# Optimization experiments

Measured on AMD Instinct MI355X. Metric: run time of the kernel, lower is better.

The kernel has to match this reference:

```python
import jax, jax.numpy as jnp
import numpy as np

N_NODES = 100000
N_EDGES = 3200000
D_IN = 64
D_OUT = 64


def setup_inputs() -> dict:
    key = jax.random.key(0)
    k0, k1, k2, k3 = jax.random.split(key, 4)
    x = jax.random.normal(k0, (N_NODES, D_IN), dtype=jnp.float32)
    edge_index = jax.random.randint(k1, (2, N_EDGES), 0, N_NODES, dtype=jnp.int64)
    edge_weight = jax.random.uniform(k2, (N_EDGES,), dtype=jnp.float32)
    W = jax.random.normal(k3, (D_IN, D_OUT), dtype=jnp.float32) / jnp.sqrt(jnp.float32(D_IN))
    b = jnp.zeros((D_OUT,), dtype=jnp.float32)
    return {"x": x, "edge_index": edge_index, "edge_weight": edge_weight, "W": W, "b": b}


def reference(x, edge_index, edge_weight, W, b):
    # GiGCNConv forward: asymmetric (random-walk, D^-1 A) gcn_norm with self loops,
    # then GCNConv(normalize=False): linear -> edge-weighted scatter-add -> bias.
    N = x.shape[0]
    src, dst = edge_index[0], edge_index[1]

    # add self loops (fill value 1.0 since improved=False)
    loop = jnp.arange(N, dtype=src.dtype)
    src = jnp.concatenate([src, loop])
    dst = jnp.concatenate([dst, loop])
    ew = jnp.concatenate([edge_weight.astype(x.dtype), jnp.ones((N,), dtype=x.dtype)])

    # asymmetric normalization: in-degree (at dst) inverse scaling
    deg = jax.ops.segment_sum(ew, dst, num_segments=N)          # [N]
    deg_inv = jnp.where(deg > 0, 1.0 / deg, 0.0)                # inf -> 0
    norm = deg_inv[dst] * ew                                    # [E+N]

    # GCNConv: project then aggregate messages at destination nodes
    h = x @ W                                                   # [N, D_OUT]
    msg = norm[:, None] * h[src]                                # [E+N, D_OUT] gather
    out = jax.ops.segment_sum(msg, dst, num_segments=N)         # scatter-add
    return out + b
```

## Files before the change

### kernel.cpp

```cpp
#include <hip/hip_runtime.h>


#define D 64
#define BSH 9
#define NPB 512
#define MAXB1 256
#define BATCHA 4096
#define C1S 32
#define WSCALE 8192.0f
#define WINV (1.0f / 8192.0f)

static __device__ __forceinline__ unsigned short f2bf(float f) {
    unsigned u = __float_as_uint(f);
    u += 0x7FFFu + ((u >> 16) & 1u);
    return (unsigned short)(u >> 16);
}
static __device__ __forceinline__ float bf2f(unsigned short s) {
    return __uint_as_float(((unsigned)s) << 16);
}


__global__ __launch_bounds__(256) void hist_kernel(const int* __restrict__ dst,
                                                   int* __restrict__ hist, int E, int B1) {
    __shared__ int lh[MAXB1];
    int tid = threadIdx.x;
    if (tid < MAXB1) lh[tid] = 0;
    __syncthreads();
    int t = blockIdx.x * 256 + tid;
    int stride = gridDim.x * 256;
    if ((E & 3) == 0 && (((size_t)dst & 15) == 0)) {
        const int4* d4 = (const int4*)dst;
        int n4 = E >> 2;
        for (int e = t; e < n4; e += stride) {
            int4 v = d4[e];
            atomicAdd(&lh[v.x >> BSH], 1);
            atomicAdd(&lh[v.y >> BSH], 1);
            atomicAdd(&lh[v.z >> BSH], 1);
            atomicAdd(&lh[v.w >> BSH], 1);
        }
    } else {
        for (int e = t; e < E; e += stride) {
            int d = __builtin_nontemporal_load(dst + e);
            atomicAdd(&lh[d >> BSH], 1);
        }
    }
    __syncthreads();
    if (tid < B1) {
        int v = lh[tid];
        if (v) atomicAdd(&hist[tid], v);
    }
}


__global__ __launch_bounds__(256) void scan_kernel(const int* __restrict__ hist,
                                                   int* __restrict__ off1,
                                                   int* __restrict__ cur1, int B1, int E) {
    __shared__ int s[256];
    int tid = threadIdx.x;
    int v = (tid < B1) ? hist[tid] : 0;
    s[tid] = v;
    __syncthreads();
    for (int o = 1; o < 256; o <<= 1) {
        int t = (tid >= o) ? s[tid - o] : 0;
        __syncthreads();
        s[tid] += t;
        __syncthreads();
    }
    if (tid < B1) {
        int ex = s[tid] - v;
        off1[tid] = ex;
        cur1[tid * C1S] = ex;
    }
    if (tid == 0) off1[B1] = E;
}


__global__ __launch_bounds__(256) void partA_kernel(const int* __restrict__ src,
                                                    const int* __restrict__ dst,
                                                    const float* __restrict__ ew,
                                                    int* __restrict__ cur1,
                                                    int2* __restrict__ pairs1,
                                                    int E, int nb, int aligned) {
    __shared__ int bcnt[MAXB1];
    __shared__ int bbase[MAXB1];
    __shared__ int brank[MAXB1];
    int tid = threadIdx.x;
    for (int ib = blockIdx.x; ib < nb; ib += gridDim.x) {
        int base = ib * BATCHA;
        int blen = E - base;
        if (blen > BATCHA) blen = BATCHA;
        if (tid < MAXB1) { bcnt[tid] = 0; brank[tid] = 0; }
        __syncthreads();
        int dv[16], sv[16];
        float wv[16];
        int off = tid * 16;
        if (aligned && off + 16 <= blen) {
#pragma unroll
            for (int kk = 0; kk < 4; ++kk) {
                int4 d4 = ((const int4*)(dst + base + off))[kk];
                int4 s4 = ((const int4*)(src + base + off))[kk];
                float4 w4 = ((const float4*)(ew + base + off))[kk];
                dv[kk * 4 + 0] = d4.x; dv[kk * 4 + 1] = d4.y;
                dv[kk * 4 + 2] = d4.z; dv[kk * 4 + 3] = d4.w;
                sv[kk * 4 + 0] = s4.x; sv[kk * 4 + 1] = s4.y;
                sv[kk * 4 + 2] = s4.z; sv[kk * 4 + 3] = s4.w;
                wv[kk * 4 + 0] = w4.x; wv[kk * 4 + 1] = w4.y;
                wv[kk * 4 + 2] = w4.z; wv[kk * 4 + 3] = w4.w;
            }
#pragma unroll
            for (int m = 0; m < 16; ++m) atomicAdd(&bcnt[dv[m] >> BSH], 1);
        } else {
#pragma unroll
            for (int m = 0; m < 16; ++m) {
                bool v = (off + m) < blen;
                int e = base + off + m;
                dv[m] = v ? __builtin_nontemporal_load(dst + e) : -1;
                sv[m] = v ? __builtin_nontemporal_load(src + e) : 0;
                wv[m] = v ? __builtin_nontemporal_load(ew + e) : 0.0f;
                if (v) atomicAdd(&bcnt[dv[m] >> BSH], 1);
            }
        }
        __syncthreads();
        if (tid < MAXB1 && bcnt[tid] > 0)
            bbase[tid] = atomicAdd(&cur1[tid * C1S], bcnt[tid]);
        __syncthreads();
#pragma unroll
        for (int m = 0; m < 16; ++m) {
            if (dv[m] >= 0) {
                int bin = dv[m] >> BSH;
                int r = atomicAdd(&brank[bin], 1);
                pairs1[bbase[bin] + r] =
                    make_int2(sv[m] | ((dv[m] & (NPB - 1)) << 17),
                              __float_as_int(wv[m]));
            }
        }
        __syncthreads();
    }
}


__global__ __launch_bounds__(512) void sortmerge_kernel(const int2* __restrict__ pairs1,
                                                        const int* __restrict__ off1,
                                                        unsigned* __restrict__ cw,
                                                        int* __restrict__ node_off,
                                                        int N, int B1) {
    __shared__ int lh[NPB];
    __shared__ int s[NPB];
    __shared__ int cur[NPB];
    int tid = threadIdx.x;
    int c = blockIdx.x;
    int e0 = off1[c], e1 = off1[c + 1];

    lh[tid] = 0;
    __syncthreads();

    for (int ib = e0; ib < e1; ib += 512 * 8) {
        long long pv[8];
#pragma unroll
        for (int m = 0; m < 8; ++m) {
            int i = ib + m * 512 + tid;
            pv[m] = (i < e1)
                ? __builtin_nontemporal_load((const long long*)(pairs1 + i))
                : -1LL;
        }
#pragma unroll
        for (int m = 0; m < 8; ++m) {
            int i = ib + m * 512 + tid;
            if (i < e1) atomicAdd(&lh[((int)pv[m] >> 17) & (NPB - 1)], 1);
        }
    }
    __syncthreads();

    s[tid] = lh[tid];
    __syncthreads();
    for (int o = 1; o < NPB; o <<= 1) {
        int t = (tid >= o) ? s[tid - o] : 0;
        __syncthreads();
        s[tid] += t;
        __syncthreads();
    }
    int ex = s[tid] - lh[tid];
    int gbase = c << BSH;
    if (gbase + tid <= N) node_off[gbase + tid] = e0 + ex;
    if (c == B1 - 1 && tid == 0) node_off[N] = e1;
    cur[tid] = ex;
    __syncthreads();

    for (int ib = e0; ib < e1; ib += 512 * 8) {
        long long pv[8];
#pragma unroll
        for (int m = 0; m < 8; ++m) {
            int i = ib + m * 512 + tid;
            pv[m] = (i < e1)
                ? __builtin_nontemporal_load((const long long*)(pairs1 + i))
                : -1LL;
        }
#pragma unroll
        for (int m = 0; m < 8; ++m) {
            int i = ib + m * 512 + tid;
            if (i < e1) {
                int px = (int)pv[m];
                float w = __int_as_float((int)(pv[m] >> 32));
                int node = (px >> 17) & (NPB - 1);
                int pos = atomicAdd(&cur[node], 1);
                int wq = (int)fminf(fmaxf(w, 0.0f) * WSCALE + 0.5f, 32767.0f);
                cw[e0 + pos] = (unsigned)(px & 0x1FFFF) | ((unsigned)wq << 17);
            }
        }
    }
}


__global__ __launch_bounds__(256) void gemmW_kernel(const float* __restrict__ x,
                                                    const float* __restrict__ W,
                                                    unsigned short* __restrict__ hbf, int N) {
    __shared__ float Ws[D * D];
    __shared__ float xs[32][D];
    int tid = threadIdx.x;
    int j = tid & 63;
    int g = tid >> 6;
    int base = blockIdx.x * 32;
    for (int i = tid; i < D * D; i += 256) Ws[i] = W[i];
    for (int rr = g; rr < 32; rr += 4) {
        int r = base + rr;
        if (r < N) xs[rr][j] = x[(size_t)r * D + j];
    }
    __syncthreads();
    float wc[D];
#pragma unroll
    for (int k = 0; k < D; ++k) wc[k] = Ws[k * D + j];
    for (int rr = g; rr < 32; rr += 4) {
        int r = base + rr;
        if (r < N) {
            float s0 = 0.0f, s1 = 0.0f, s2 = 0.0f, s3 = 0.0f;
#pragma unroll
            for (int k = 0; k < D; k += 4) {
                s0 = fmaf(xs[rr][k + 0], wc[k + 0], s0);
                s1 = fmaf(xs[rr][k + 1], wc[k + 1], s1);
                s2 = fmaf(xs[rr][k + 2], wc[k + 2], s2);
                s3 = fmaf(xs[rr][k + 3], wc[k + 3], s3);
            }
            hbf[(size_t)r * D + j] = f2bf((s0 + s1) + (s2 + s3));
        }
    }
}


__global__ __launch_bounds__(256) void accum_kernel(const unsigned* __restrict__ cw,
                                                    const int* __restrict__ node_off,
                                                    const unsigned short* __restrict__ hbf,
                                                    const float* __restrict__ bias,
                                                    float* __restrict__ out, int N) {
    int t = blockIdx.x * 256 + threadIdx.x;
    int n = t >> 6;
    int j = t & 63;
    if (n >= N) return;
    float acc = bf2f(hbf[(size_t)n * D + j]);
    float degs = 1.0f;
    int base = node_off[n];
    int cnt = node_off[n + 1] - base;
    const unsigned* pp = cw + base;
    int i = 0;
    for (; i + 7 < cnt; i += 8) {
        unsigned v0 = pp[i + 0];
        unsigned v1 = pp[i + 1];
        unsigned v2 = pp[i + 2];
        unsigned v3 = pp[i + 3];
        unsigned v4 = pp[i + 4];
        unsigned v5 = pp[i + 5];
        unsigned v6 = pp[i + 6];
        unsigned v7 = pp[i + 7];
        float h0 = bf2f(hbf[(size_t)(v0 & 0x1FFFF) * D + j]);
        float h1 = bf2f(hbf[(size_t)(v1 & 0x1FFFF) * D + j]);
        float h2 = bf2f(hbf[(size_t)(v2 & 0x1FFFF) * D + j]);
        float h3 = bf2f(hbf[(size_t)(v3 & 0x1FFFF) * D + j]);
        float h4 = bf2f(hbf[(size_t)(v4 & 0x1FFFF) * D + j]);
        float h5 = bf2f(hbf[(size_t)(v5 & 0x1FFFF) * D + j]);
        float h6 = bf2f(hbf[(size_t)(v6 & 0x1FFFF) * D + j]);
        float h7 = bf2f(hbf[(size_t)(v7 & 0x1FFFF) * D + j]);
        float w0 = (float)(v0 >> 17) * WINV;
        float w1 = (float)(v1 >> 17) * WINV;
        float w2 = (float)(v2 >> 17) * WINV;
        float w3 = (float)(v3 >> 17) * WINV;
        float w4 = (float)(v4 >> 17) * WINV;
        float w5 = (float)(v5 >> 17) * WINV;
        float w6 = (float)(v6 >> 17) * WINV;
        float w7 = (float)(v7 >> 17) * WINV;
        degs += ((w0 + w1) + (w2 + w3)) + ((w4 + w5) + (w6 + w7));
        acc = fmaf(w0, h0, acc);
        acc = fmaf(w1, h1, acc);
        acc = fmaf(w2, h2, acc);
        acc = fmaf(w3, h3, acc);
        acc = fmaf(w4, h4, acc);
        acc = fmaf(w5, h5, acc);
        acc = fmaf(w6, h6, acc);
        acc = fmaf(w7, h7, acc);
    }
    for (; i < cnt; ++i) {
        unsigned v = pp[i];
        float w = (float)(v >> 17) * WINV;
        degs += w;
        acc = fmaf(w, bf2f(hbf[(size_t)(v & 0x1FFFF) * D + j]), acc);
    }
    float di = (degs > 0.0f) ? (1.0f / degs) : 0.0f;
    __builtin_nontemporal_store(fmaf(di, acc, bias[j]), &out[(size_t)n * D + j]);
}


__global__ __launch_bounds__(256) void deg_kernel(const int* __restrict__ dst,
                                                  const float* __restrict__ ew,
                                                  float* __restrict__ deg, int E) {
    int t = blockIdx.x * 256 + threadIdx.x;
    int stride = gridDim.x * 256;
    for (int e = t; e < E; e += stride) atomicAdd(&deg[dst[e]], ew[e]);
}

__global__ __launch_bounds__(256) void deginv_kernel(float* __restrict__ deg, int N) {
    int t = blockIdx.x * 256 + threadIdx.x;
    int stride = gridDim.x * 256;
    for (int n = t; n < N; n += stride) {
        float tot = deg[n] + 1.0f;
        deg[n] = (tot > 0.0f) ? (1.0f / tot) : 0.0f;
    }
}

__global__ __launch_bounds__(256) void gemm16f_kernel(const float* __restrict__ x,
                                                      const float* __restrict__ W,
                                                      float* __restrict__ h, int N) {
    __shared__ float Ws[D * D];
    __shared__ float xs[16][D];
    int tid = threadIdx.x;
    int j = tid & 63;
    int q = tid >> 6;
    int base = blockIdx.x * 16;
    for (int i = tid; i < D * D; i += 256) Ws[i] = W[i];
    for (int rr = q; rr < 16; rr += 4) {
        int r = base + rr;
        if (r < N) xs[rr][j] = x[(size_t)r * D + j];
    }
    __syncthreads();
    for (int rr = q; rr < 16; rr += 4) {
        int r = base + rr;
        if (r < N) {
            float sum = 0.0f;
#pragma unroll
            for (int k = 0; k < D; ++k) sum = fmaf(xs[rr][k], Ws[k * D + j], sum);
            h[(size_t)r * D + j] = sum;
        }
    }
}

__global__ __launch_bounds__(256) void init_kernel(const float* __restrict__ h,
                                                   const float* __restrict__ deginv,
                                                   const float* __restrict__ b,
                                                   float* __restrict__ out, int N) {
    int t = blockIdx.x * 256 + threadIdx.x;
    int stride = gridDim.x * 256;
    int nq = N * (D / 4);
    const float4* h4 = (const float4*)h;
    const float4* b4 = (const float4*)b;
    float4* o4 = (float4*)out;
    for (int q = t; q < nq; q += stride) {
        int n = q >> 4;
        int c4 = q & 15;
        float4 hv = h4[q];
        float4 bv = b4[c4];
        float di = deginv[n];
        float4 o;
        o.x = bv.x + di * hv.x;
        o.y = bv.y + di * hv.y;
        o.z = bv.z + di * hv.z;
        o.w = bv.w + di * hv.w;
        o4[q] = o;
    }
}

__global__ __launch_bounds__(256) void scatter_kernel(const int* __restrict__ src,
                                                      const int* __restrict__ dst,
                                                      const float* __restrict__ ew,
                                                      const float* __restrict__ deginv,
                                                      const float* __restrict__ h,
                                                      float* __restrict__ out, int E) {
    int t = blockIdx.x * 256 + threadIdx.x;
    int wave = t >> 6;
    int lane = t & 63;
    int nwaves = (gridDim.x * 256) >> 6;
    for (int e = wave; e < E; e += nwaves) {
        int s = src[e];
        int d = dst[e];
        float norm = deginv[d] * ew[e];
        atomicAdd(&out[d * D + lane], norm * h[s * D + lane]);
    }
}


extern "C" void kernel_launch(void* const* d_in, const int* in_sizes, int n_in,
                              void* d_out, int out_size, void* d_ws, size_t ws_size,
                              hipStream_t stream) {
    const float* x  = (const float*)d_in[0];
    const int*   ei = (const int*)d_in[1];
    const float* ew = (const float*)d_in[2];
    const float* W  = (const float*)d_in[3];
    const float* b  = (const float*)d_in[4];
    float* out = (float*)d_out;

    int N = in_sizes[0] / D;
    int E = in_sizes[2];
    const int* srcp = ei;
    const int* dstp = ei + E;

    int B1 = (N + NPB - 1) >> BSH;

    size_t ints_n = 256 + 320 + (size_t)MAXB1 * C1S + ((size_t)N + 64);
    size_t p1_off  = ((ints_n * 4) + 255) & ~(size_t)255;
    size_t hbf_off = (p1_off + (size_t)E * 8 + 255) & ~(size_t)255;
    size_t cw_off  = (hbf_off + (size_t)N * D * 2 + 255) & ~(size_t)255;
    size_t need = cw_off + (size_t)E * 4;

    if (N <= 131072 && ws_size >= need) {
        int* hist     = (int*)d_ws;
        int* off1     = hist + 256;
        int* cur1     = off1 + 320;
        int* node_off = cur1 + (size_t)MAXB1 * C1S;
        int2* pairs1  = (int2*)((char*)d_ws + p1_off);
        unsigned short* hbf = (unsigned short*)((char*)d_ws + hbf_off);
        unsigned* cw  = (unsigned*)((char*)d_ws + cw_off);

        int aligned = (((E & 3) == 0) && (((size_t)dstp & 15) == 0)) ? 1 : 0;

        hipMemsetAsync(hist, 0, 256 * 4, stream);
        hist_kernel<<<512, 256, 0, stream>>>(dstp, hist, E, B1);
        scan_kernel<<<1, 256, 0, stream>>>(hist, off1, cur1, B1, E);
        int nb = (E + BATCHA - 1) / BATCHA;
        int gA = nb < 2048 ? nb : 2048;
        partA_kernel<<<gA, 256, 0, stream>>>(srcp, dstp, ew, cur1, pairs1, E, nb, aligned);
        sortmerge_kernel<<<B1, 512, 0, stream>>>(pairs1, off1, cw, node_off, N, B1);
        gemmW_kernel<<<(N + 31) / 32, 256, 0, stream>>>(x, W, hbf, N);
        accum_kernel<<<(N + 3) / 4, 256, 0, stream>>>(cw, node_off, hbf, b, out, N);
    } else {
        size_t Npad = ((size_t)N + 63) & ~(size_t)63;
        float* deg = (float*)d_ws;
        float* h = deg + Npad;
        hipMemsetAsync(deg, 0, (size_t)N * sizeof(float), stream);
        deg_kernel<<<2048, 256, 0, stream>>>(dstp, ew, deg, E);
        deginv_kernel<<<(N + 255) / 256, 256, 0, stream>>>(deg, N);
        gemm16f_kernel<<<(N + 15) / 16, 256, 0, stream>>>(x, W, h, N);
        init_kernel<<<2048, 256, 0, stream>>>(h, deg, b, out, N);
        scatter_kernel<<<2048, 256, 0, stream>>>(srcp, dstp, ew, deg, h, out, E);
    }
}
```

Baseline: 208.4 us.

## Split node wavefront into four edge groups with 4-wide bf16 gathers and shuffle reduction

The accumulate kernel now gives each 64-lane wavefront four edge groups of 16 lanes. Each lane loads 4 bf16 features as a uint2, so one edge row is read with 8-byte loads, and each lane walks a strided subset of the node's edges. Partial sums and degrees are combined with xor-shuffles, and only the first group adds the self-loop term and bias and writes the output. The aim is wider gathers and more edges in flight per wavefront. The cost is shuffle overhead, three quarters of the lanes sitting idle during the final write, and a changed floating-point summation order.

```diff
diff --git a/kernel.cpp b/kernel.cpp
--- a/kernel.cpp
+++ b/kernel.cpp
@@ -17,6 +17,12 @@
 }
 static __device__ __forceinline__ float bf2f(unsigned short s) {
     return __uint_as_float(((unsigned)s) << 16);
+}
+static __device__ __forceinline__ float bflo(unsigned u) {
+    return __uint_as_float(u << 16);
+}
+static __device__ __forceinline__ float bfhi(unsigned u) {
+    return __uint_as_float(u & 0xFFFF0000u);
 }
 
 
@@ -253,57 +259,74 @@
                                                     float* __restrict__ out, int N) {
     int t = blockIdx.x * 256 + threadIdx.x;
     int n = t >> 6;
-    int j = t & 63;
+    int l = t & 63;
     if (n >= N) return;
-    float acc = bf2f(hbf[(size_t)n * D + j]);
-    float degs = 1.0f;
+    int eg = l >> 4;
+    int cl = l & 15;
     int base = node_off[n];
     int cnt = node_off[n + 1] - base;
     const unsigned* pp = cw + base;
-    int i = 0;
-    for (; i + 7 < cnt; i += 8) {
-        unsigned v0 = pp[i + 0];
-        unsigned v1 = pp[i + 1];
-        unsigned v2 = pp[i + 2];
-        unsigned v3 = pp[i + 3];
-        unsigned v4 = pp[i + 4];
-        unsigned v5 = pp[i + 5];
-        unsigned v6 = pp[i + 6];
-        unsigned v7 = pp[i + 7];
-        float h0 = bf2f(hbf[(size_t)(v0 & 0x1FFFF) * D + j]);
-        float h1 = bf2f(hbf[(size_t)(v1 & 0x1FFFF) * D + j]);
-        float h2 = bf2f(hbf[(size_t)(v2 & 0x1FFFF) * D + j]);
-        float h3 = bf2f(hbf[(size_t)(v3 & 0x1FFFF) * D + j]);
-        float h4 = bf2f(hbf[(size_t)(v4 & 0x1FFFF) * D + j]);
-        float h5 = bf2f(hbf[(size_t)(v5 & 0x1FFFF) * D + j]);
-        float h6 = bf2f(hbf[(size_t)(v6 & 0x1FFFF) * D + j]);
-        float h7 = bf2f(hbf[(size_t)(v7 & 0x1FFFF) * D + j]);
-        float w0 = (float)(v0 >> 17) * WINV;
-        float w1 = (float)(v1 >> 17) * WINV;
-        float w2 = (float)(v2 >> 17) * WINV;
-        float w3 = (float)(v3 >> 17) * WINV;
-        float w4 = (float)(v4 >> 17) * WINV;
-        float w5 = (float)(v5 >> 17) * WINV;
-        float w6 = (float)(v6 >> 17) * WINV;
-        float w7 = (float)(v7 >> 17) * WINV;
-        degs += ((w0 + w1) + (w2 + w3)) + ((w4 + w5) + (w6 + w7));
-        acc = fmaf(w0, h0, acc);
-        acc = fmaf(w1, h1, acc);
-        acc = fmaf(w2, h2, acc);
-        acc = fmaf(w3, h3, acc);
-        acc = fmaf(w4, h4, acc);
-        acc = fmaf(w5, h5, acc);
-        acc = fmaf(w6, h6, acc);
-        acc = fmaf(w7, h7, acc);
-    }
-    for (; i < cnt; ++i) {
+    const unsigned short* hcol = hbf + cl * 4;
+
+    float a0 = 0.0f, a1 = 0.0f, a2 = 0.0f, a3 = 0.0f;
+    float degs = 0.0f;
+    int i = eg;
+    for (; i + 4 < cnt; i += 8) {
+        unsigned va = pp[i];
+        unsigned vb = pp[i + 4];
+        unsigned sa = va & 0x1FFFF;
+        unsigned sb = vb & 0x1FFFF;
+        uint2 ha = *(const uint2*)(hcol + (size_t)sa * D);
+        uint2 hb = *(const uint2*)(hcol + (size_t)sb * D);
+        float wa = (float)(va >> 17) * WINV;
+        float wb = (float)(vb >> 17) * WINV;
+        degs += wa + wb;
+        a0 = fmaf(wa, bflo(ha.x), a0);
+        a1 = fmaf(wa, bfhi(ha.x), a1);
+        a2 = fmaf(wa, bflo(ha.y), a2);
+        a3 = fmaf(wa, bfhi(ha.y), a3);
+        a0 = fmaf(wb, bflo(hb.x), a0);
+        a1 = fmaf(wb, bfhi(hb.x), a1);
+        a2 = fmaf(wb, bflo(hb.y), a2);
+        a3 = fmaf(wb, bfhi(hb.y), a3);
+    }
+    if (i < cnt) {
         unsigned v = pp[i];
+        unsigned s = v & 0x1FFFF;
+        uint2 hv = *(const uint2*)(hcol + (size_t)s * D);
         float w = (float)(v >> 17) * WINV;
         degs += w;
-        acc = fmaf(w, bf2f(hbf[(size_t)(v & 0x1FFFF) * D + j]), acc);
-    }
-    float di = (degs > 0.0f) ? (1.0f / degs) : 0.0f;
-    __builtin_nontemporal_store(fmaf(di, acc, bias[j]), &out[(size_t)n * D + j]);
+        a0 = fmaf(w, bflo(hv.x), a0);
+        a1 = fmaf(w, bfhi(hv.x), a1);
+        a2 = fmaf(w, bflo(hv.y), a2);
+        a3 = fmaf(w, bfhi(hv.y), a3);
+    }
+
+    a0 += __shfl_xor(a0, 16); a0 += __shfl_xor(a0, 32);
+    a1 += __shfl_xor(a1, 16); a1 += __shfl_xor(a1, 32);
+    a2 += __shfl_xor(a2, 16); a2 += __shfl_xor(a2, 32);
+    a3 += __shfl_xor(a3, 16); a3 += __shfl_xor(a3, 32);
+    degs += __shfl_xor(degs, 16); degs += __shfl_xor(degs, 32);
+
+    if (eg == 0) {
+        uint2 hs = *(const uint2*)(hcol + (size_t)n * D);
+        a0 += bflo(hs.x);
+        a1 += bfhi(hs.x);
+        a2 += bflo(hs.y);
+        a3 += bfhi(hs.y);
+        degs += 1.0f;
+        float di = 1.0f / degs;
+        const float4 bv = *(const float4*)(bias + cl * 4);
+        float4 o;
+        o.x = fmaf(di, a0, bv.x);
+        o.y = fmaf(di, a1, bv.y);
+        o.z = fmaf(di, a2, bv.z);
+        o.w = fmaf(di, a3, bv.w);
+        __builtin_nontemporal_store(o.x, out + (size_t)n * D + cl * 4 + 0);
+        __builtin_nontemporal_store(o.y, out + (size_t)n * D + cl * 4 + 1);
+        __builtin_nontemporal_store(o.z, out + (size_t)n * D + cl * 4 + 2);
+        __builtin_nontemporal_store(o.w, out + (size_t)n * D + cl * 4 + 3);
+    }
 }
 
 
```

Result: faster. 188.8 us (-9.4%).
